# Performance work log

Measured on AMD Instinct MI355X. Metric: run time of the kernel, lower is better.

Reference implementation:

```python
import jax, jax.numpy as jnp
import numpy as np

PH, PW = 7, 7
SPATIAL_SCALE = 0.0625


def _hat_int(t):
    # Antiderivative of the unit hat (triangle) function phi(t)=max(0,1-|t|),
    # i.e. integral_{-inf}^{t} phi. Piecewise quadratic, saturates to [0,1].
    t = jnp.clip(t, -1.0, 1.0)
    return jnp.where(t <= 0, 0.5 * (t + 1.0) ** 2, 1.0 - 0.5 * (1.0 - t) ** 2)


def _bin_weights(lo, hi, size):
    # lo, hi: [R, P] continuous bin boundaries (in feature-map coordinates).
    # Returns [R, P, size]: exact 1D integral of the hat basis at each integer
    # grid node over [lo, hi]. Bilinear interpolation is the tensor product of
    # 1D hat bases, so the exact 2D PrRoI integral separates into these weights.
    grid = jnp.arange(size, dtype=lo.dtype)
    return _hat_int(hi[..., None] - grid) - _hat_int(lo[..., None] - grid)


def _prroi_pool(features, rois):
    N, C, H, W = features.shape
    R = rois.shape[0]
    dt = features.dtype
    bidx = rois[:, 0].astype(jnp.int32)
    x1 = rois[:, 1] * SPATIAL_SCALE
    y1 = rois[:, 2] * SPATIAL_SCALE
    x2 = rois[:, 3] * SPATIAL_SCALE
    y2 = rois[:, 4] * SPATIAL_SCALE
    roi_w = jnp.maximum(x2 - x1, 0.0)
    roi_h = jnp.maximum(y2 - y1, 0.0)
    bw = roi_w / PW  # [R]
    bh = roi_h / PH
    px = jnp.arange(PW, dtype=dt)
    py = jnp.arange(PH, dtype=dt)
    x_lo = x1[:, None] + px[None, :] * bw[:, None]  # [R, PW]
    x_hi = x_lo + bw[:, None]
    y_lo = y1[:, None] + py[None, :] * bh[:, None]  # [R, PH]
    y_hi = y_lo + bh[:, None]
    Wx = _bin_weights(x_lo, x_hi, W)  # [R, PW, W]
    Wy = _bin_weights(y_lo, y_hi, H)  # [R, PH, H]
    area = bw * bh  # [R]
    inv_area = jnp.where(area > 0, 1.0 / jnp.maximum(area, 1e-12), 0.0)
    out = jnp.zeros((R, C, PH, PW), dtype=dt)
    for n in range(N):  # small fixed batch loop; avoids [R,C,H,W] gather
        m = (bidx == n).astype(dt)
        out = out + jnp.einsum('rph,chw,rqw->rcpq', Wy * m[:, None, None], features[n], Wx)
    return out * inv_area[:, None, None, None]


def setup_inputs() -> dict:
    key = jax.random.key(0)
    k1, k2, k3, k4, k5, k6 = jax.random.split(key, 6)
    N, C, H, W, R = 2, 256, 152, 152, 512
    features = jax.random.normal(k1, (N, C, H, W), dtype=jnp.float32)
    img = H / SPATIAL_SCALE  # 2432 px image
    bidx = jax.random.randint(k2, (R,), 0, N).astype(jnp.float32)
    x1 = jax.random.uniform(k3, (R,), minval=0.0, maxval=img * 0.7)
    y1 = jax.random.uniform(k4, (R,), minval=0.0, maxval=img * 0.7)
    x2 = x1 + jax.random.uniform(k5, (R,), minval=32.0, maxval=img * 0.3)
    y2 = y1 + jax.random.uniform(k6, (R,), minval=32.0, maxval=img * 0.3)
    rois = jnp.stack([bidx, x1, y1, x2, y2], axis=1).astype(jnp.float32)
    return {"features": features, "rois": rois}


def reference(features, rois):
    return _prroi_pool(features, rois)
```

## Files before the change

### kernel.cpp

```cpp
#include <hip/hip_runtime.h>

#define PHH 7
#define PWW 7
#define WXW 48
static constexpr float SPATIAL_SCALE = 0.0625f;

__device__ __forceinline__ float hat_int(float t) {
    t = fminf(fmaxf(t, -1.0f), 1.0f);
    float a = t + 1.0f, b = 1.0f - t;
    return (t <= 0.0f) ? 0.5f * a * a : 1.0f - 0.5f * b * b;
}

__device__ __forceinline__ float bin_w(float lo, float hi, float g) {
    return hat_int(hi - g) - hat_int(lo - g);
}

__device__ __forceinline__ unsigned short f32_to_bf16_rne(float x) {
    unsigned int u = __float_as_uint(x);
    unsigned int r = 0x7FFFu + ((u >> 16) & 1u);
    return (unsigned short)((u + r) >> 16);
}

__device__ __forceinline__ float bf_lo(unsigned int v) {
    return __uint_as_float(v << 16);
}
__device__ __forceinline__ float bf_hi(unsigned int v) {
    return __uint_as_float(v & 0xFFFF0000u);
}

__global__ __launch_bounds__(256) void transpose_nchw_nhwc_bf16_v2(
    const float* __restrict__ src, unsigned short* __restrict__ dst,
    int C, int HW)
{
    __shared__ unsigned short tile[64][66];
    const int n = blockIdx.z;
    const int hw0 = blockIdx.x * 64;
    const int c0 = blockIdx.y * 64;
    const float* s = src + (size_t)n * C * HW;
    unsigned short* d = dst + (size_t)n * C * HW;

    const int tx = threadIdx.x & 63;
    const int ty = threadIdx.x >> 6;
    #pragma unroll
    for (int i = 0; i < 16; ++i) {
        const int cl = ty * 16 + i;
        const int c = c0 + cl, hw = hw0 + tx;
        if (c < C && hw < HW)
            tile[cl][tx] = f32_to_bf16_rne(s[(size_t)c * HW + hw]);
    }
    __syncthreads();

    const int cl = threadIdx.x & 31;
    const int hb = threadIdx.x >> 5;
    #pragma unroll
    for (int i = 0; i < 8; ++i) {
        const int hwl = hb * 8 + i;
        const int hw = hw0 + hwl;
        const int c = c0 + 2 * cl;
        if (hw < HW && c < C) {
            const unsigned int v = (unsigned int)tile[2 * cl][hwl]
                                 | ((unsigned int)tile[2 * cl + 1][hwl] << 16);
            *(unsigned int*)(d + (size_t)hw * C + c) = v;
        }
    }
}

__global__ __launch_bounds__(128) void prroi_weights(
    const float* __restrict__ rois, float* __restrict__ wx,
    float* __restrict__ wys, int H, int W, int R)
{
    const int r = blockIdx.x;
    const float* roi = rois + (size_t)r * 5;
    const float x1 = roi[1] * SPATIAL_SCALE;
    const float y1 = roi[2] * SPATIAL_SCALE;
    const float x2 = roi[3] * SPATIAL_SCALE;
    const float y2 = roi[4] * SPATIAL_SCALE;
    const float bw = fmaxf(x2 - x1, 0.0f) / (float)PWW;
    const float bh = fmaxf(y2 - y1, 0.0f) / (float)PHH;
    const float area = bw * bh;
    const float inv_area = (area > 0.0f) ? 1.0f / fmaxf(area, 1e-12f) : 0.0f;
    const int w0 = max(0, (int)ceilf(x1 - 1.0f));
    const int w1 = min(W - 1, (int)floorf(x2 + 1.0f));
    const int ww = min(w1 - w0 + 1, WXW);

    const int tid = threadIdx.x;
    if (tid < WXW) {
        const float g = (float)(w0 + tid);
        float* o = wx + ((size_t)r * WXW + tid) * 8;
        #pragma unroll
        for (int q = 0; q < PWW; ++q) {
            const float lo = x1 + (float)q * bw;
            o[q] = (tid < ww) ? bin_w(lo, lo + bw, g) * inv_area : 0.0f;
        }
        o[7] = 0.0f;
    }
    if (tid < PHH * 16) {
        const int p = tid >> 4;
        const int i = tid & 15;
        const float ylo = y1 + (float)p * bh;
        const float yhi = ylo + bh;
        const int h0 = max(0, (int)ceilf(ylo - 1.0f));
        const int h1 = min(H - 1, (int)floorf(yhi + 1.0f));
        const int nh = min(h1 - h0 + 1, 16);
        wys[((size_t)r * PHH + p) * 16 + i] =
            (i < nh) ? bin_w(ylo, yhi, (float)(h0 + i)) : 0.0f;
    }
}

__global__ __launch_bounds__(128) void prroi_pool_nolds(
    const unsigned short* __restrict__ ft,
    const float* __restrict__ rois,
    const float* __restrict__ wx,
    const float* __restrict__ wys,
    float* __restrict__ out,
    int H, int W, int R)
{
    const int nwg = R * PHH;
    int task = (int)blockIdx.x;
    if ((nwg & 7) == 0) {
        const int cpx = nwg >> 3;
        task = (task & 7) * cpx + (task >> 3);
    }
    const int r = task / PHH;
    const int p = task % PHH;

    const int chHalf = threadIdx.x >> 6;
    const int lane = threadIdx.x & 63;
    const int c0 = chHalf * 128 + lane * 2;

    const float* roi = rois + (size_t)r * 5;
    const int b = (int)roi[0];
    const float x1 = roi[1] * SPATIAL_SCALE;
    const float y1 = roi[2] * SPATIAL_SCALE;
    const float x2 = roi[3] * SPATIAL_SCALE;
    const float y2 = roi[4] * SPATIAL_SCALE;
    const float bh = fmaxf(y2 - y1, 0.0f) / (float)PHH;

    const float ylo = y1 + (float)p * bh;
    const float yhi = ylo + bh;
    const int h0 = max(0, (int)ceilf(ylo - 1.0f));
    const int h1 = min(H - 1, (int)floorf(yhi + 1.0f));
    const int w0 = max(0, (int)ceilf(x1 - 1.0f));
    const int w1 = min(W - 1, (int)floorf(x2 + 1.0f));
    const int nh = min(h1 - h0 + 1, 16);
    const int ww = min(w1 - w0 + 1, WXW);

    const float* wysr = wys + ((size_t)r * PHH + p) * 16;
    const float* wxr = wx + (size_t)r * WXW * 8;

    float acc[PWW][2];
    #pragma unroll
    for (int q = 0; q < PWW; ++q) { acc[q][0] = 0.0f; acc[q][1] = 0.0f; }

    const size_t rowstride = (size_t)W * 256;
    const unsigned short* base =
        ft + ((size_t)b * H + (size_t)h0) * rowstride + (size_t)w0 * 256 + c0;

    for (int chunk = 0; chunk < ww; chunk += 8) {
        int off[8];
        #pragma unroll
        for (int j = 0; j < 8; ++j)
            off[j] = (chunk + j < ww) ? (chunk + j) * 256 : 0;

        float u[2][8];
        #pragma unroll
        for (int j = 0; j < 8; ++j) { u[0][j] = 0.0f; u[1][j] = 0.0f; }

        auto load_row = [&](unsigned int (&v)[8], int i) {
            const unsigned short* rp = base + (size_t)i * rowstride;
            #pragma unroll
            for (int j = 0; j < 8; ++j)
                v[j] = *(const unsigned int*)(rp + off[j]);
        };
        auto fma_row = [&](const unsigned int (&v)[8], float wy) {
            #pragma unroll
            for (int j = 0; j < 8; ++j) {
                u[0][j] = fmaf(wy, bf_lo(v[j]), u[0][j]);
                u[1][j] = fmaf(wy, bf_hi(v[j]), u[1][j]);
            }
        };

        unsigned int A[8], B[8], C[8];
        load_row(A, 0);
        if (nh > 1) load_row(B, 1);
        int i = 0;
        while (true) {
            if (i + 2 < nh) load_row(C, i + 2);
            fma_row(A, wysr[i]);
            if (++i >= nh) break;
            if (i + 2 < nh) load_row(A, i + 2);
            fma_row(B, wysr[i]);
            if (++i >= nh) break;
            if (i + 2 < nh) load_row(B, i + 2);
            fma_row(C, wysr[i]);
            if (++i >= nh) break;
        }

        #pragma unroll
        for (int j = 0; j < 8; ++j) {
            const float4 wa = *(const float4*)&wxr[(chunk + j) * 8];
            const float4 wb = *(const float4*)&wxr[(chunk + j) * 8 + 4];
            acc[0][0] = fmaf(wa.x, u[0][j], acc[0][0]);
            acc[0][1] = fmaf(wa.x, u[1][j], acc[0][1]);
            acc[1][0] = fmaf(wa.y, u[0][j], acc[1][0]);
            acc[1][1] = fmaf(wa.y, u[1][j], acc[1][1]);
            acc[2][0] = fmaf(wa.z, u[0][j], acc[2][0]);
            acc[2][1] = fmaf(wa.z, u[1][j], acc[2][1]);
            acc[3][0] = fmaf(wa.w, u[0][j], acc[3][0]);
            acc[3][1] = fmaf(wa.w, u[1][j], acc[3][1]);
            acc[4][0] = fmaf(wb.x, u[0][j], acc[4][0]);
            acc[4][1] = fmaf(wb.x, u[1][j], acc[4][1]);
            acc[5][0] = fmaf(wb.y, u[0][j], acc[5][0]);
            acc[5][1] = fmaf(wb.y, u[1][j], acc[5][1]);
            acc[6][0] = fmaf(wb.z, u[0][j], acc[6][0]);
            acc[6][1] = fmaf(wb.z, u[1][j], acc[6][1]);
        }
    }

    float* o = out + ((size_t)r * 256 + c0) * (PHH * PWW) + p * PWW;
    #pragma unroll
    for (int q = 0; q < PWW; ++q) {
        o[q]             = acc[q][0];
        o[PHH * PWW + q] = acc[q][1];
    }
}

__global__ __launch_bounds__(256) void prroi_pool_nchw(
    const float* __restrict__ f, const float* __restrict__ rois,
    float* __restrict__ out, int C, int H, int W, int R)
{
    const int idx = blockIdx.x * blockDim.x + threadIdx.x;
    const int total = R * C * PHH * PWW;
    if (idx >= total) return;
    const int q = idx % PWW;
    const int p = (idx / PWW) % PHH;
    const int c = (idx / (PWW * PHH)) % C;
    const int r = idx / (PWW * PHH * C);
    const float* roi = rois + (size_t)r * 5;
    const int b = (int)roi[0];
    const float x1 = roi[1] * SPATIAL_SCALE;
    const float y1 = roi[2] * SPATIAL_SCALE;
    const float x2 = roi[3] * SPATIAL_SCALE;
    const float y2 = roi[4] * SPATIAL_SCALE;
    const float bw = fmaxf(x2 - x1, 0.0f) / (float)PWW;
    const float bh = fmaxf(y2 - y1, 0.0f) / (float)PHH;
    const float area = bw * bh;
    const float inv_area = (area > 0.0f) ? 1.0f / fmaxf(area, 1e-12f) : 0.0f;
    const float xlo = x1 + (float)q * bw, xhi = xlo + bw;
    const float ylo = y1 + (float)p * bh, yhi = ylo + bh;
    const int h0 = max(0, (int)ceilf(ylo - 1.0f));
    const int h1 = min(H - 1, (int)floorf(yhi + 1.0f));
    const int w0 = max(0, (int)ceilf(xlo - 1.0f));
    const int w1 = min(W - 1, (int)floorf(xhi + 1.0f));
    float acc = 0.0f;
    for (int h = h0; h <= h1; ++h) {
        const float wy = bin_w(ylo, yhi, (float)h);
        const float* fr = f + (((size_t)b * C + c) * H + h) * W;
        for (int w = w0; w <= w1; ++w)
            acc = fmaf(wy * bin_w(xlo, xhi, (float)w), fr[w], acc);
    }
    out[idx] = acc * inv_area;
}

extern "C" void kernel_launch(void* const* d_in, const int* in_sizes, int n_in,
                              void* d_out, int out_size, void* d_ws, size_t ws_size,
                              hipStream_t stream)
{
    const float* features = (const float*)d_in[0];
    const float* rois = (const float*)d_in[1];
    float* out = (float*)d_out;

    const int C = 256, H = 152, W = 152;
    const int N = in_sizes[0] / (C * H * W);
    const int R = in_sizes[1] / 5;

    const size_t ft_bytes = (size_t)N * C * H * W * sizeof(unsigned short);
    const size_t wx_off = ft_bytes;
    const size_t wys_off = wx_off + (size_t)R * WXW * 8 * 4;
    const size_t need = wys_off + (size_t)R * PHH * 16 * 4;

    if (ws_size >= need && C == 256) {
        unsigned short* ft = (unsigned short*)d_ws;
        float* wx = (float*)((char*)d_ws + wx_off);
        float* wys = (float*)((char*)d_ws + wys_off);
        const int HW = H * W;
        dim3 tgrid((HW + 63) / 64, (C + 63) / 64, N);
        transpose_nchw_nhwc_bf16_v2<<<tgrid, 256, 0, stream>>>(features, ft, C, HW);
        prroi_weights<<<R, 128, 0, stream>>>(rois, wx, wys, H, W, R);
        prroi_pool_nolds<<<R * PHH, 128, 0, stream>>>(ft, rois, wx, wys, out, H, W, R);
    } else {
        const int total = R * C * PHH * PWW;
        prroi_pool_nchw<<<(total + 255) / 256, 256, 0, stream>>>(features, rois, out, C, H, W, R);
    }
}
```

Baseline: 61.15 us.

## Fuse ROI weight computation into transpose kernel and batch row loads by four

Merges the separate ROI weight kernel into the NCHW-to-NHWC bf16 transpose kernel, so the first R blocks also compute the wx/wys tables and one launch is removed. The pool kernel replaces its three-buffer rolling row pipeline with groups of four row loads issued together, clamping row indices and relying on zero-padded wy weights past nh. It also adds a minimum-occupancy hint to the pool kernel's launch bounds. In exchange, the transpose blocks that handle weights do extra work, redundant clamped rows are loaded, and the occupancy hint may cause register spills.

```diff
diff --git a/kernel.cpp b/kernel.cpp
--- a/kernel.cpp
+++ b/kernel.cpp
@@ -28,10 +28,50 @@
     return __uint_as_float(v & 0xFFFF0000u);
 }
 
-__global__ __launch_bounds__(256) void transpose_nchw_nhwc_bf16_v2(
+__global__ __launch_bounds__(256) void transpose_weights(
     const float* __restrict__ src, unsigned short* __restrict__ dst,
-    int C, int HW)
-{
+    const float* __restrict__ rois, float* __restrict__ wx,
+    float* __restrict__ wys, int C, int HW, int H, int W, int R)
+{
+    const int bid = (int)blockIdx.x +
+                    (int)gridDim.x * ((int)blockIdx.y + (int)gridDim.y * (int)blockIdx.z);
+    const int tid = threadIdx.x;
+    if (bid < R && tid < 112) {
+        const float* roi = rois + (size_t)bid * 5;
+        const float x1 = roi[1] * SPATIAL_SCALE;
+        const float y1 = roi[2] * SPATIAL_SCALE;
+        const float x2 = roi[3] * SPATIAL_SCALE;
+        const float y2 = roi[4] * SPATIAL_SCALE;
+        const float bw = fmaxf(x2 - x1, 0.0f) / (float)PWW;
+        const float bh = fmaxf(y2 - y1, 0.0f) / (float)PHH;
+        const float area = bw * bh;
+        const float inv_area = (area > 0.0f) ? 1.0f / fmaxf(area, 1e-12f) : 0.0f;
+        if (tid < WXW) {
+            const int w0 = max(0, (int)ceilf(x1 - 1.0f));
+            const int w1 = min(W - 1, (int)floorf(x2 + 1.0f));
+            const int ww = min(w1 - w0 + 1, WXW);
+            const float g = (float)(w0 + tid);
+            float* o = wx + ((size_t)bid * WXW + tid) * 8;
+            #pragma unroll
+            for (int q = 0; q < PWW; ++q) {
+                const float lo = x1 + (float)q * bw;
+                o[q] = (tid < ww) ? bin_w(lo, lo + bw, g) * inv_area : 0.0f;
+            }
+            o[7] = 0.0f;
+        }
+        {
+            const int p = tid >> 4;
+            const int i = tid & 15;
+            const float ylo = y1 + (float)p * bh;
+            const float yhi = ylo + bh;
+            const int h0 = max(0, (int)ceilf(ylo - 1.0f));
+            const int h1 = min(H - 1, (int)floorf(yhi + 1.0f));
+            const int nh = min(h1 - h0 + 1, 16);
+            wys[((size_t)bid * PHH + p) * 16 + i] =
+                (i < nh) ? bin_w(ylo, yhi, (float)(h0 + i)) : 0.0f;
+        }
+    }
+
     __shared__ unsigned short tile[64][66];
     const int n = blockIdx.z;
     const int hw0 = blockIdx.x * 64;
@@ -65,49 +105,7 @@
     }
 }
 
-__global__ __launch_bounds__(128) void prroi_weights(
-    const float* __restrict__ rois, float* __restrict__ wx,
-    float* __restrict__ wys, int H, int W, int R)
-{
-    const int r = blockIdx.x;
-    const float* roi = rois + (size_t)r * 5;
-    const float x1 = roi[1] * SPATIAL_SCALE;
-    const float y1 = roi[2] * SPATIAL_SCALE;
-    const float x2 = roi[3] * SPATIAL_SCALE;
-    const float y2 = roi[4] * SPATIAL_SCALE;
-    const float bw = fmaxf(x2 - x1, 0.0f) / (float)PWW;
-    const float bh = fmaxf(y2 - y1, 0.0f) / (float)PHH;
-    const float area = bw * bh;
-    const float inv_area = (area > 0.0f) ? 1.0f / fmaxf(area, 1e-12f) : 0.0f;
-    const int w0 = max(0, (int)ceilf(x1 - 1.0f));
-    const int w1 = min(W - 1, (int)floorf(x2 + 1.0f));
-    const int ww = min(w1 - w0 + 1, WXW);
-
-    const int tid = threadIdx.x;
-    if (tid < WXW) {
-        const float g = (float)(w0 + tid);
-        float* o = wx + ((size_t)r * WXW + tid) * 8;
-        #pragma unroll
-        for (int q = 0; q < PWW; ++q) {
-            const float lo = x1 + (float)q * bw;
-            o[q] = (tid < ww) ? bin_w(lo, lo + bw, g) * inv_area : 0.0f;
-        }
-        o[7] = 0.0f;
-    }
-    if (tid < PHH * 16) {
-        const int p = tid >> 4;
-        const int i = tid & 15;
-        const float ylo = y1 + (float)p * bh;
-        const float yhi = ylo + bh;
-        const int h0 = max(0, (int)ceilf(ylo - 1.0f));
-        const int h1 = min(H - 1, (int)floorf(yhi + 1.0f));
-        const int nh = min(h1 - h0 + 1, 16);
-        wys[((size_t)r * PHH + p) * 16 + i] =
-            (i < nh) ? bin_w(ylo, yhi, (float)(h0 + i)) : 0.0f;
-    }
-}
-
-__global__ __launch_bounds__(128) void prroi_pool_nolds(
+__global__ __launch_bounds__(128, 4) void prroi_pool_nolds(
     const unsigned short* __restrict__ ft,
     const float* __restrict__ rois,
     const float* __restrict__ wx,
@@ -143,6 +141,7 @@
     const int w0 = max(0, (int)ceilf(x1 - 1.0f));
     const int w1 = min(W - 1, (int)floorf(x2 + 1.0f));
     const int nh = min(h1 - h0 + 1, 16);
+    const int nh4 = (nh + 3) & ~3;
     const int ww = min(w1 - w0 + 1, WXW);
 
     const float* wysr = wys + ((size_t)r * PHH + p) * 16;
@@ -155,6 +154,7 @@
     const size_t rowstride = (size_t)W * 256;
     const unsigned short* base =
         ft + ((size_t)b * H + (size_t)h0) * rowstride + (size_t)w0 * 256 + c0;
+    const int nhm1 = nh - 1;
 
     for (int chunk = 0; chunk < ww; chunk += 8) {
         int off[8];
@@ -166,34 +166,24 @@
         #pragma unroll
         for (int j = 0; j < 8; ++j) { u[0][j] = 0.0f; u[1][j] = 0.0f; }
 
-        auto load_row = [&](unsigned int (&v)[8], int i) {
-            const unsigned short* rp = base + (size_t)i * rowstride;
+        for (int i = 0; i < nh4; i += 4) {
+            unsigned int v[4][8];
             #pragma unroll
-            for (int j = 0; j < 8; ++j)
-                v[j] = *(const unsigned int*)(rp + off[j]);
-        };
-        auto fma_row = [&](const unsigned int (&v)[8], float wy) {
+            for (int k = 0; k < 4; ++k) {
+                const unsigned short* rp = base + (size_t)min(i + k, nhm1) * rowstride;
+                #pragma unroll
+                for (int j = 0; j < 8; ++j)
+                    v[k][j] = *(const unsigned int*)(rp + off[j]);
+            }
             #pragma unroll
-            for (int j = 0; j < 8; ++j) {
-                u[0][j] = fmaf(wy, bf_lo(v[j]), u[0][j]);
-                u[1][j] = fmaf(wy, bf_hi(v[j]), u[1][j]);
+            for (int k = 0; k < 4; ++k) {
+                const float wy = wysr[i + k];
+                #pragma unroll
+                for (int j = 0; j < 8; ++j) {
+                    u[0][j] = fmaf(wy, bf_lo(v[k][j]), u[0][j]);
+                    u[1][j] = fmaf(wy, bf_hi(v[k][j]), u[1][j]);
+                }
             }
-        };
-
-        unsigned int A[8], B[8], C[8];
-        load_row(A, 0);
-        if (nh > 1) load_row(B, 1);
-        int i = 0;
-        while (true) {
-            if (i + 2 < nh) load_row(C, i + 2);
-            fma_row(A, wysr[i]);
-            if (++i >= nh) break;
-            if (i + 2 < nh) load_row(A, i + 2);
-            fma_row(B, wysr[i]);
-            if (++i >= nh) break;
-            if (i + 2 < nh) load_row(B, i + 2);
-            fma_row(C, wysr[i]);
-            if (++i >= nh) break;
         }
 
         #pragma unroll
@@ -285,8 +275,8 @@
         float* wys = (float*)((char*)d_ws + wys_off);
         const int HW = H * W;
         dim3 tgrid((HW + 63) / 64, (C + 63) / 64, N);
-        transpose_nchw_nhwc_bf16_v2<<<tgrid, 256, 0, stream>>>(features, ft, C, HW);
-        prroi_weights<<<R, 128, 0, stream>>>(rois, wx, wys, H, W, R);
+        transpose_weights<<<tgrid, 256, 0, stream>>>(
+            features, ft, rois, wx, wys, C, HW, H, W, R);
         prroi_pool_nolds<<<R * PHH, 128, 0, stream>>>(ft, rois, wx, wys, out, H, W, R);
     } else {
         const int total = R * C * PHH * PWW;
```

Result: faster. 56.05 us (-8.3%).
